# Performance work log

Measured on AMD Instinct MI355X. Metric: run time of the kernel, lower is better.

Reference implementation:

```python
import jax, jax.numpy as jnp
import numpy as np

DIM = 2048          # SDR dimension
CTX = 512           # top-down context (grid code) dimension
B = 8192            # batch of independent samples
N_PV = DIM // 4     # 512 PV interneurons
N_SV = DIM // 8     # 256 SOM/VIP interneurons
ALPHA_POS = 1.0 / 10.0   # dt / tau_pos
ALPHA_NEG = 1.0 / 10.0   # dt / tau_neg


def setup_inputs() -> dict:
    key = jax.random.key(0)
    ks = jax.random.split(key, 14)
    sc = 1.0 / np.sqrt(DIM)
    sc_sv = 1.0 / np.sqrt(N_SV)
    xav = np.sqrt(6.0 / (CTX + DIM))  # xavier uniform bound for predictor
    u = lambda k, shp, s: jax.random.uniform(k, shp, dtype=jnp.float32) * s
    return {
        "x_batch": jax.random.uniform(ks[0], (B, DIM), dtype=jnp.float32),
        "context_batch": jax.random.normal(ks[1], (B, CTX), dtype=jnp.float32),
        "r_pos_batch": jax.random.uniform(ks[2], (B, DIM), dtype=jnp.float32),
        "r_neg_batch": jax.random.uniform(ks[3], (B, DIM), dtype=jnp.float32),
        "W_pred": jax.random.uniform(ks[4], (DIM, CTX), jnp.float32, -xav, xav),
        "b_pred": jnp.zeros((DIM,), jnp.float32),
        "W_pv1_ff": u(ks[5], (N_PV, DIM), sc),
        "W_pv2_td": u(ks[6], (N_PV, DIM), sc),
        "W_vip_td": u(ks[7], (N_SV, DIM), sc),
        "W_som_in": u(ks[8], (N_SV, DIM), sc),
        "W_vip_som": u(ks[9], (N_SV, N_SV), sc_sv),
        "W_inh_pe_pos": u(ks[10], (DIM, N_PV), sc),
        "W_inh_pe_neg": u(ks[11], (DIM, N_PV), sc),
        "W_som_dend": u(ks[12], (DIM, N_SV), sc),
    }


def reference(x_batch, context_batch, r_pos_batch, r_neg_batch,
              W_pred, b_pred, W_pv1_ff, W_pv2_td, W_vip_td, W_som_in,
              W_vip_som, W_inh_pe_pos, W_inh_pe_neg, W_som_dend):
    relu = jax.nn.relu
    # top-down prediction: (B, CTX) @ (CTX, DIM) -> (B, DIM)
    predicted = context_batch @ W_pred.T + b_pred
    # interneuron circuit (Nemati 2025)
    r_pv1 = relu(x_batch @ W_pv1_ff.T)                               # (B, N_PV)
    r_pv2 = relu(predicted @ W_pv2_td.T)                             # (B, N_PV)
    r_vip = relu(predicted @ W_vip_td.T)                             # (B, N_SV)
    r_som = relu(relu(x_batch @ W_som_in.T) - r_vip @ W_vip_som.T)   # (B, N_SV)
    # signed prediction errors with somatic/dendritic inhibition
    pe_pos = relu(x_batch - predicted - r_pv2 @ W_inh_pe_pos.T)
    pe_neg = relu(predicted - x_batch - r_pv1 @ W_inh_pe_neg.T - r_som @ W_som_dend.T)
    # low-pass temporal filter of PE states
    new_r_pos = (1.0 - ALPHA_POS) * r_pos_batch + ALPHA_POS * pe_pos
    new_r_neg = (1.0 - ALPHA_NEG) * r_neg_batch + ALPHA_NEG * pe_neg
    return (new_r_pos, new_r_neg)
```

## Files before the change

kernel.cpp:

```cpp
#include <hip/hip_runtime.h>
#include <hip/hip_bf16.h>
#include <stdint.h>
#include <stddef.h>

#define DIMV 2048
#define CTXV 512
#define BV   8192
#define NPV  512
#define NSV  256

typedef __attribute__((ext_vector_type(8))) __bf16 bf16x8;
typedef __attribute__((ext_vector_type(4))) __bf16 bf16x4;
typedef __attribute__((ext_vector_type(4))) float f32x4;

__device__ __forceinline__ void gload_lds16(const void* g, void* l) {
    __builtin_amdgcn_global_load_lds(
        (const __attribute__((address_space(1))) unsigned int*)g,
        (__attribute__((address_space(3))) unsigned int*)l,
        16, 0, 0);
}

#define WAIT_VM8  asm volatile("s_waitcnt vmcnt(8)" ::: "memory")
#define WAIT_VM4  asm volatile("s_waitcnt vmcnt(4)" ::: "memory")
#define WAIT_VM0  asm volatile("s_waitcnt vmcnt(0)" ::: "memory")
#define WAIT_LGKM asm volatile("s_waitcnt lgkmcnt(0)" ::: "memory")
#define SBAR      __builtin_amdgcn_s_barrier()
#define SCHEDB    __builtin_amdgcn_sched_barrier(0)

struct CvtArgs {
    const float* src[11];
    __bf16*      dst[11];
};

__global__ __launch_bounds__(256) void cvt_all(CvtArgs a) {
    constexpr int NSEG = 11;
    constexpr unsigned cum[NSEG + 1] = {
        0u, 2097152u, 2621440u, 2752512u, 2883584u, 3014656u,
        3080192u, 3145728u, 3153920u, 3284992u, 3416064u, 3481600u};
    const unsigned total = cum[NSEG];
    for (unsigned c = blockIdx.x * blockDim.x + threadIdx.x; c < total;
         c += gridDim.x * blockDim.x) {
        const float* sp = a.src[0];
        __bf16*      dp = a.dst[0];
        unsigned     base = 0;
#pragma unroll
        for (int t = 1; t < NSEG; ++t) {
            const bool g = (c >= cum[t]);
            sp   = g ? a.src[t] : sp;
            dp   = g ? a.dst[t] : dp;
            base = g ? cum[t] : base;
        }
        const unsigned off = (c - base) * 8u;
        f32x4 v0 = *(const f32x4*)(sp + off);
        f32x4 v1 = *(const f32x4*)(sp + off + 4);
        bf16x8 o;
#pragma unroll
        for (int e = 0; e < 4; ++e) { o[e] = (__bf16)v0[e]; o[e + 4] = (__bf16)v1[e]; }
        *(bf16x8*)(dp + off) = o;
    }
}

__global__ __launch_bounds__(256)
void cvtT_wpred(const float* __restrict__ W, __bf16* __restrict__ WT) {
    __shared__ float t[64 * 65];
    const int bi  = blockIdx.x & 31;
    const int bj  = blockIdx.x >> 5;
    const int tid = threadIdx.x;
    const int tr  = tid >> 4;
    const int tc  = tid & 15;
#pragma unroll
    for (int rr = 0; rr < 4; ++rr) {
        const int r = tr + rr * 16;
        f32x4 v = *(const f32x4*)(W + (size_t)(bi * 64 + r) * 512 + bj * 64 + tc * 4);
#pragma unroll
        for (int e = 0; e < 4; ++e) t[(tc * 4 + e) * 65 + r] = v[e];
    }
    __syncthreads();
#pragma unroll
    for (int rr = 0; rr < 4; ++rr) {
        const int c = tr + rr * 16;
        bf16x4 o;
#pragma unroll
        for (int e = 0; e < 4; ++e) o[e] = (__bf16)t[c * 65 + tc * 4 + e];
        *(bf16x4*)(WT + (size_t)(bj * 64 + c) * 2048 + bi * 64 + tc * 4) = o;
    }
}

__global__ __launch_bounds__(512)
void bias_comb(const __bf16* __restrict__ Wpv2, const __bf16* __restrict__ Wvip,
               const float* __restrict__ b, float* __restrict__ out) {
    const int tid  = threadIdx.x;
    const int gw   = blockIdx.x * 8 + (tid >> 6);
    const int lane = tid & 63;
    const __bf16* row = (gw < 512) ? (Wpv2 + (size_t)gw * 2048)
                                   : (Wvip + (size_t)(gw - 512) * 2048);
    float acc = 0.f;
#pragma unroll
    for (int c = 0; c < 4; ++c) {
        const int j = lane * 32 + c * 8;
        bf16x8 w = *(const bf16x8*)(row + j);
        f32x4 b0 = *(const f32x4*)(b + j);
        f32x4 b1 = *(const f32x4*)(b + j + 4);
#pragma unroll
        for (int e = 0; e < 4; ++e) acc += (float)w[e] * b0[e];
#pragma unroll
        for (int e = 0; e < 4; ++e) acc += (float)w[e + 4] * b1[e];
    }
#pragma unroll
    for (int off = 32; off > 0; off >>= 1) acc += __shfl_down(acc, off);
    if (lane == 0) out[gw] = acc;
}

struct GemmDesc {
    const __bf16* A; int ldA;
    const __bf16* W1; const __bf16* W2; int ldW;
    int NB1;
    int N1cols, N2cols;
    int K, ntN;
    int epi;
    const float* bias;
    const __bf16* subp;
    void* out1; void* out2;
};

#define GEOM4                                                     \
    const int tid  = threadIdx.x;                                 \
    const int wave = tid >> 6;                                    \
    const int lane = tid & 63;                                    \
    const int lhi  = lane >> 4;                                   \
    const int llo  = lane & 15;                                   \
    const int wr   = wave >> 1;                                   \
    const int wc   = wave & 1;                                    \
    const int rins = lane >> 2;                                   \
    const int ch   = lane & 3;

#define LOAD_FRAGS5(BUF, af, bfr)                                     \
    _Pragma("unroll")                                                 \
    for (int i = 0; i < 4; ++i) {                                     \
        const int r  = wr * 64 + i * 16 + llo;                        \
        const int pc = lhi ^ ((r >> 1) & 3);                          \
        af[i] = *(const bf16x8*)(&ldsA[BUF][r * 64 + pc * 16]);       \
    }                                                                 \
    _Pragma("unroll")                                                 \
    for (int j = 0; j < 4; ++j) {                                     \
        const int r  = wc * 64 + j * 16 + llo;                        \
        const int pc = lhi ^ ((r >> 1) & 3);                          \
        bfr[j] = *(const bf16x8*)(&ldsB[BUF][r * 64 + pc * 16]);      \
    }

#define MFMA16(af, bfr, acc)                                                          \
    __builtin_amdgcn_s_setprio(1);                                                    \
    _Pragma("unroll")                                                                 \
    for (int i = 0; i < 4; ++i)                                                       \
        _Pragma("unroll")                                                             \
        for (int j = 0; j < 4; ++j)                                                   \
            acc[i][j] = __builtin_amdgcn_mfma_f32_16x16x32_bf16(bfr[j], af[i], acc[i][j], 0, 0, 0); \
    __builtin_amdgcn_s_setprio(0);

__global__ __launch_bounds__(256, 3)
void pe_gemm5(GemmDesc dA_, GemmDesc dB_, GemmDesc dC_, int s1, int s2)
{
    __shared__ __align__(16) char ldsA[3][8192];
    __shared__ __align__(16) char ldsB[3][8192];

    const int nwg = gridDim.x;
    const int bid = blockIdx.x;
    int wg = (bid & 7) * (nwg >> 3) + (bid >> 3);
    GemmDesc d = dA_;
    if (wg >= s2)      { d = dC_; wg -= s2; }
    else if (wg >= s1) { d = dB_; wg -= s1; }

    const int bx = wg / d.ntN;
    const int by = wg - bx * d.ntN;
    const int m0 = bx * 128;
    const int n0 = by * 128;

    const bool reg2  = (n0 >= d.NB1);
    const __bf16* Wc = reg2 ? d.W2 : d.W1;
    const int n0r    = reg2 ? (n0 - d.NB1) : n0;

    GEOM4

    const f32x4 fzero = {0.f, 0.f, 0.f, 0.f};
    f32x4 acc[4][4];
#pragma unroll
    for (int i = 0; i < 4; ++i)
#pragma unroll
        for (int j = 0; j < 4; ++j) acc[i][j] = fzero;

    const int nsteps = d.K >> 5;

#define STAGE5(S, BUF)                                                        \
    {                                                                         \
        const int kb_ = (S) * 32;                                             \
        _Pragma("unroll")                                                     \
        for (int half = 0; half < 2; ++half) {                                \
            const int rt = wave * 32 + half * 16 + rins;                      \
            const int kc = ch ^ ((rt >> 1) & 3);                              \
            const int kk = kb_ + kc * 8;                                      \
            gload_lds16(d.A + (size_t)(m0 + rt) * d.ldA + kk,                 \
                        &ldsA[BUF][wave * 2048 + half * 1024]);               \
            gload_lds16(Wc + (size_t)(n0r + rt) * d.ldW + kk,                 \
                        &ldsB[BUF][wave * 2048 + half * 1024]);               \
        }                                                                     \
    }

    STAGE5(0, 0)
    if (nsteps > 1) STAGE5(1, 1)
    for (int s = 0; s < nsteps; ++s) {
        if (s + 2 < nsteps) { STAGE5(s + 2, (s + 2) % 3) WAIT_VM8; }
        else if (s + 1 < nsteps) { WAIT_VM4; }
        else { WAIT_VM0; }
        SBAR;
        const int cb = s % 3;
        bf16x8 af[4], bfr[4];
        LOAD_FRAGS5(cb, af, bfr)
        MFMA16(af, bfr, acc)
        WAIT_LGKM; SCHEDB;
        SBAR;
    }
#undef STAGE5

#pragma unroll
    for (int i = 0; i < 4; ++i) {
#pragma unroll
        for (int j = 0; j < 4; ++j) {
            const int rowg = m0 + wr * 64 + i * 16 + llo;
            const int colb = wc * 64 + j * 16 + lhi * 4;
            if (d.epi == 0) {
                const size_t idx = (size_t)rowg * d.N1cols + (n0 + colb);
                f32x4 b4 = *(const f32x4*)(d.bias + n0 + colb);
                bf16x4 o;
#pragma unroll
                for (int r = 0; r < 4; ++r) o[r] = (__bf16)(acc[i][j][r] + b4[r]);
                *(bf16x4*)((__bf16*)d.out1 + idx) = o;
            } else if (d.epi == 1) {
                __bf16* op    = reg2 ? (__bf16*)d.out2 : (__bf16*)d.out1;
                const int ldo = reg2 ? d.N2cols : d.N1cols;
                const size_t idx = (size_t)rowg * ldo + (n0r + colb);
                bf16x4 o;
#pragma unroll
                for (int r = 0; r < 4; ++r) o[r] = (__bf16)fmaxf(acc[i][j][r], 0.f);
                *(bf16x4*)(op + idx) = o;
            } else if (d.epi == 2) {
                const size_t idx = (size_t)rowg * d.N1cols + (n0 + colb);
                bf16x4 s4 = *(const bf16x4*)(d.subp + idx);
                bf16x4 o;
#pragma unroll
                for (int r = 0; r < 4; ++r)
                    o[r] = (__bf16)fmaxf((float)s4[r] - acc[i][j][r], 0.f);
                *(bf16x4*)((__bf16*)d.out1 + idx) = o;
            } else if (d.epi == 3) {
                const size_t idx = (size_t)rowg * d.N1cols + (n0 + colb);
                bf16x4 o;
#pragma unroll
                for (int r = 0; r < 4; ++r) o[r] = (__bf16)acc[i][j][r];
                *(bf16x4*)((__bf16*)d.out1 + idx) = o;
            } else {
                __bf16* op    = reg2 ? (__bf16*)d.out2 : (__bf16*)d.out1;
                const int ldo = reg2 ? d.N2cols : d.N1cols;
                const size_t idx = (size_t)rowg * ldo + (n0r + colb);
                f32x4 b4 = *(const f32x4*)(d.bias + n0 + colb);
                bf16x4 o;
#pragma unroll
                for (int r = 0; r < 4; ++r)
                    o[r] = (__bf16)fmaxf(acc[i][j][r] + b4[r], 0.f);
                *(bf16x4*)(op + idx) = o;
            }
        }
    }
}

__global__ __launch_bounds__(256, 3)
void pe_filt5(const __bf16* __restrict__ rpv2, const __bf16* __restrict__ Wpepos,
              const __bf16* __restrict__ rpv1, const __bf16* __restrict__ rsom,
              const __bf16* __restrict__ Wpeneg, const __bf16* __restrict__ Wsomd,
              const __bf16* __restrict__ xbf, const __bf16* __restrict__ predb,
              const float* __restrict__ rpos, const float* __restrict__ rneg,
              float* __restrict__ outp, float* __restrict__ outn)
{
    __shared__ __align__(16) char ldsA[3][8192];
    __shared__ __align__(16) char ldsB[3][8192];

    const int nwg = gridDim.x;
    const int bid = blockIdx.x;
    const int wg  = (bid & 7) * (nwg >> 3) + (bid >> 3);
    const int bx  = wg >> 4;
    const int by  = wg & 15;
    const int m0  = bx * 128;
    const int n0  = by * 128;

    GEOM4

#define STAGE_F(Asrc, ldAv, Wsrc, ldWv, KB, BUF)                              \
    {                                                                         \
        _Pragma("unroll")                                                     \
        for (int half = 0; half < 2; ++half) {                                \
            const int rt = wave * 32 + half * 16 + rins;                      \
            const int kc = ch ^ ((rt >> 1) & 3);                              \
            const int kk = (KB) + kc * 8;                                     \
            gload_lds16((Asrc) + (size_t)(m0 + rt) * (ldAv) + kk,             \
                        &ldsA[BUF][wave * 2048 + half * 1024]);               \
            gload_lds16((Wsrc) + (size_t)(n0 + rt) * (ldWv) + kk,             \
                        &ldsB[BUF][wave * 2048 + half * 1024]);               \
        }                                                                     \
    }
#define STAGE_NEG(S, BUF)                                                     \
    {                                                                         \
        if ((S) < 16) { STAGE_F(rpv1, NPV, Wpeneg, NPV, (S) * 32, BUF) }      \
        else          { STAGE_F(rsom, NSV, Wsomd, NSV, ((S) - 16) * 32, BUF) }\
    }

    const f32x4 fzero = {0.f, 0.f, 0.f, 0.f};
    f32x4 acc[4][4];
#pragma unroll
    for (int i = 0; i < 4; ++i)
#pragma unroll
        for (int j = 0; j < 4; ++j) acc[i][j] = fzero;

    STAGE_F(rpv2, NPV, Wpepos, NPV, 0, 0)
    STAGE_F(rpv2, NPV, Wpepos, NPV, 32, 1)
    for (int s = 0; s < 16; ++s) {
        if (s + 2 < 16) { STAGE_F(rpv2, NPV, Wpepos, NPV, (s + 2) * 32, (s + 2) % 3) WAIT_VM8; }
        else if (s + 1 < 16) { WAIT_VM4; }
        else { WAIT_VM0; }
        SBAR;
        const int cb = s % 3;
        bf16x8 af[4], bfr[4];
        LOAD_FRAGS5(cb, af, bfr)
        MFMA16(af, bfr, acc)
        WAIT_LGKM; SCHEDB;
        SBAR;
    }
    STAGE_NEG(0, 0)
    STAGE_NEG(1, 1)

#pragma unroll
    for (int i = 0; i < 4; ++i) {
#pragma unroll
        for (int j = 0; j < 4; ++j) {
            const int rowg = m0 + wr * 64 + i * 16 + llo;
            const int colg = n0 + wc * 64 + j * 16 + lhi * 4;
            const size_t idx = (size_t)rowg * 2048 + colg;
            f32x4 rp  = *(const f32x4*)(rpos + idx);
            bf16x4 xb = *(const bf16x4*)(xbf + idx);
            bf16x4 pb = *(const bf16x4*)(predb + idx);
            f32x4 o;
#pragma unroll
            for (int r = 0; r < 4; ++r) {
                const float dd = (float)xb[r] - (float)pb[r];
                o[r] = 0.9f * rp[r] + 0.1f * fmaxf(dd - acc[i][j][r], 0.f);
            }
            *(f32x4*)(outp + idx) = o;
            acc[i][j] = fzero;
        }
    }

    for (int s = 0; s < 24; ++s) {
        if (s + 2 < 24) { STAGE_NEG(s + 2, (s + 2) % 3) WAIT_VM8; }
        else if (s + 1 < 24) { WAIT_VM4; }
        else { WAIT_VM0; }
        SBAR;
        const int cb = s % 3;
        bf16x8 af[4], bfr[4];
        LOAD_FRAGS5(cb, af, bfr)
        MFMA16(af, bfr, acc)
        WAIT_LGKM; SCHEDB;
        SBAR;
    }

#pragma unroll
    for (int i = 0; i < 4; ++i) {
#pragma unroll
        for (int j = 0; j < 4; ++j) {
            const int rowg = m0 + wr * 64 + i * 16 + llo;
            const int colg = n0 + wc * 64 + j * 16 + lhi * 4;
            const size_t idx = (size_t)rowg * 2048 + colg;
            f32x4 rn  = *(const f32x4*)(rneg + idx);
            bf16x4 xb = *(const bf16x4*)(xbf + idx);
            bf16x4 pb = *(const bf16x4*)(predb + idx);
            f32x4 o;
#pragma unroll
            for (int r = 0; r < 4; ++r) {
                const float dd = (float)pb[r] - (float)xb[r];
                o[r] = 0.9f * rn[r] + 0.1f * fmaxf(dd - acc[i][j][r], 0.f);
            }
            *(f32x4*)(outn + idx) = o;
        }
    }
#undef STAGE_NEG
#undef STAGE_F
}

extern "C" void kernel_launch(void* const* d_in, const int* in_sizes, int n_in,
                              void* d_out, int out_size, void* d_ws, size_t ws_size,
                              hipStream_t stream) {
    (void)in_sizes; (void)n_in; (void)out_size; (void)ws_size;

    const float* x       = (const float*)d_in[0];
    const float* ctx     = (const float*)d_in[1];
    const float* r_pos   = (const float*)d_in[2];
    const float* r_neg   = (const float*)d_in[3];
    const float* Wpred   = (const float*)d_in[4];
    const float* bpred   = (const float*)d_in[5];
    const float* Wpv1    = (const float*)d_in[6];
    const float* Wpv2    = (const float*)d_in[7];
    const float* Wvip    = (const float*)d_in[8];
    const float* Wsomin  = (const float*)d_in[9];
    const float* Wvipsom = (const float*)d_in[10];
    const float* Wpepos  = (const float*)d_in[11];
    const float* Wpeneg  = (const float*)d_in[12];
    const float* Wsomd   = (const float*)d_in[13];

    char* ws = (char*)d_ws;
    __bf16* x_bf      = (__bf16*)ws; ws += (size_t)BV * DIMV * 2;
    __bf16* ctx_bf    = (__bf16*)ws; ws += (size_t)BV * CTXV * 2;
    __bf16* pred_bf   = (__bf16*)ws; ws += (size_t)BV * DIMV * 2;
    __bf16* rpv1_bf   = (__bf16*)ws; ws += (size_t)BV * NPV * 2;
    __bf16* rpv2_bf   = (__bf16*)ws; ws += (size_t)BV * NPV * 2;
    __bf16* rvip_bf   = (__bf16*)ws; ws += (size_t)BV * NSV * 2;
    __bf16* ssom_bf   = (__bf16*)ws; ws += (size_t)BV * NSV * 2;
    __bf16* rsom_bf   = (__bf16*)ws; ws += (size_t)BV * NSV * 2;
    __bf16* Wpred_bf  = (__bf16*)ws; ws += (size_t)DIMV * CTXV * 2;
    __bf16* Wpv1_bf   = (__bf16*)ws; ws += (size_t)NPV * DIMV * 2;
    __bf16* Wpv2_bf   = (__bf16*)ws; ws += (size_t)NPV * DIMV * 2;
    __bf16* Wvip_bf   = (__bf16*)ws; ws += (size_t)NSV * DIMV * 2;
    __bf16* Wsomin_bf = (__bf16*)ws; ws += (size_t)NSV * DIMV * 2;
    __bf16* Wvipsom_bf= (__bf16*)ws; ws += (size_t)NSV * NSV * 2;
    __bf16* Wpepos_bf = (__bf16*)ws; ws += (size_t)DIMV * NPV * 2;
    __bf16* Wpeneg_bf = (__bf16*)ws; ws += (size_t)DIMV * NPV * 2;
    __bf16* Wsomd_bf  = (__bf16*)ws; ws += (size_t)DIMV * NSV * 2;
    __bf16* WpredT_bf = (__bf16*)ws; ws += (size_t)CTXV * DIMV * 2;
    __bf16* Wcomb2    = (__bf16*)ws; ws += (size_t)NPV * CTXV * 2;
    __bf16* Wcombv    = (__bf16*)ws; ws += (size_t)NSV * CTXV * 2;
    float*  biascomb  = (float*)ws;  ws += 768 * 4;

    float* out_pos = (float*)d_out;
    float* out_neg = out_pos + (size_t)BV * DIMV;

    CvtArgs ca;
    ca.src[0] = x;       ca.dst[0] = x_bf;
    ca.src[1] = ctx;     ca.dst[1] = ctx_bf;
    ca.src[2] = Wpred;   ca.dst[2] = Wpred_bf;
    ca.src[3] = Wpv1;    ca.dst[3] = Wpv1_bf;
    ca.src[4] = Wpv2;    ca.dst[4] = Wpv2_bf;
    ca.src[5] = Wvip;    ca.dst[5] = Wvip_bf;
    ca.src[6] = Wsomin;  ca.dst[6] = Wsomin_bf;
    ca.src[7] = Wvipsom; ca.dst[7] = Wvipsom_bf;
    ca.src[8] = Wpepos;  ca.dst[8] = Wpepos_bf;
    ca.src[9] = Wpeneg;  ca.dst[9] = Wpeneg_bf;
    ca.src[10] = Wsomd;  ca.dst[10] = Wsomd_bf;
    cvt_all<<<dim3(2048), dim3(256), 0, stream>>>(ca);
    cvtT_wpred<<<dim3(256), dim3(256), 0, stream>>>(Wpred, WpredT_bf);
    bias_comb<<<dim3(96), dim3(512), 0, stream>>>(Wpv2_bf, Wvip_bf, bpred, biascomb);

    const int BIG = 1 << 28;
    GemmDesc dz;
    dz.A = nullptr; dz.ldA = 0; dz.W1 = dz.W2 = nullptr; dz.ldW = 0;
    dz.NB1 = BIG; dz.N1cols = dz.N2cols = 0; dz.K = 32; dz.ntN = 1;
    dz.epi = 3; dz.bias = nullptr; dz.subp = nullptr;
    dz.out1 = dz.out2 = nullptr;

    GemmDesc d_pred = dz;
    d_pred.A = ctx_bf; d_pred.ldA = CTXV;
    d_pred.W1 = d_pred.W2 = Wpred_bf; d_pred.ldW = CTXV;
    d_pred.K = CTXV; d_pred.ntN = 16; d_pred.N1cols = DIMV; d_pred.epi = 0;
    d_pred.bias = bpred; d_pred.out1 = pred_bf;

    GemmDesc d_c2 = dz;
    d_c2.A = Wpv2_bf; d_c2.ldA = DIMV;
    d_c2.W1 = d_c2.W2 = WpredT_bf; d_c2.ldW = DIMV;
    d_c2.K = DIMV; d_c2.ntN = 4; d_c2.N1cols = CTXV; d_c2.epi = 3;
    d_c2.out1 = Wcomb2;

    GemmDesc d_cv = d_c2;
    d_cv.A = Wvip_bf;
    d_cv.out1 = Wcombv;

    pe_gemm5<<<dim3(1048), dim3(256), 0, stream>>>(d_pred, d_c2, d_cv, 1024, 1040);

    GemmDesc d_23 = dz;
    d_23.A = x_bf; d_23.ldA = DIMV;
    d_23.W1 = Wpv1_bf; d_23.W2 = Wsomin_bf; d_23.ldW = DIMV;
    d_23.K = DIMV; d_23.ntN = 6; d_23.NB1 = NPV;
    d_23.N1cols = NPV; d_23.N2cols = NSV; d_23.epi = 1;
    d_23.out1 = rpv1_bf; d_23.out2 = ssom_bf;

    GemmDesc d_45 = dz;
    d_45.A = ctx_bf; d_45.ldA = CTXV;
    d_45.W1 = Wcomb2; d_45.W2 = Wcombv; d_45.ldW = CTXV;
    d_45.K = CTXV; d_45.ntN = 6; d_45.NB1 = NPV;
    d_45.N1cols = NPV; d_45.N2cols = NSV; d_45.epi = 4;
    d_45.bias = biascomb; d_45.out1 = rpv2_bf; d_45.out2 = rvip_bf;

    pe_gemm5<<<dim3(768), dim3(256), 0, stream>>>(d_23, d_45, dz, 384, 768);

    GemmDesc d_som = dz;
    d_som.A = rvip_bf; d_som.ldA = NSV;
    d_som.W1 = d_som.W2 = Wvipsom_bf; d_som.ldW = NSV;
    d_som.K = NSV; d_som.ntN = 2; d_som.N1cols = NSV; d_som.epi = 2;
    d_som.subp = ssom_bf; d_som.out1 = rsom_bf;

    pe_gemm5<<<dim3(128), dim3(256), 0, stream>>>(d_som, d_som, d_som, 128, 128);

    pe_filt5<<<dim3(1024), dim3(256), 0, stream>>>(
        rpv2_bf, Wpepos_bf, rpv1_bf, rsom_bf, Wpeneg_bf, Wsomd_bf,
        x_bf, pred_bf, r_pos, r_neg, out_pos, out_neg);
}
```

Before: 313.7 us.

## Use single barrier per K-step with asm LDS reads in triple-buffered GEMM loops

Restructures the triple-buffered K loops so each step waits on the oldest prefetch, takes one barrier, then issues the next global-to-LDS prefetch before reading fragments. The trailing barrier is removed, which the 3-buffer rotation allows because the buffer being overwritten was consumed two steps earlier. LDS fragment reads become inline-asm ds_read_b128 followed by an lgkmcnt wait before the MFMAs. This aims to halve barrier overhead per step, at the cost of less compiler freedom to interleave LDS reads with MFMAs and a shallower vmcnt wait window.

After: 306.1 us. 2.4% less time.

```diff
diff --git a/kernel.cpp b/kernel.cpp
--- a/kernel.cpp
+++ b/kernel.cpp
@@ -12,6 +12,8 @@
 typedef __attribute__((ext_vector_type(8))) __bf16 bf16x8;
 typedef __attribute__((ext_vector_type(4))) __bf16 bf16x4;
 typedef __attribute__((ext_vector_type(4))) float f32x4;
+typedef __attribute__((ext_vector_type(4))) int   i32x4;
+typedef __attribute__((address_space(3))) const char* lds_cp;
 
 __device__ __forceinline__ void gload_lds16(const void* g, void* l) {
     __builtin_amdgcn_global_load_lds(
@@ -20,7 +22,12 @@
         16, 0, 0);
 }
 
-#define WAIT_VM8  asm volatile("s_waitcnt vmcnt(8)" ::: "memory")
+__device__ __forceinline__ bf16x8 lds_read16(const char* p) {
+    i32x4 r;
+    asm volatile("ds_read_b128 %0, %1" : "=v"(r) : "v"((lds_cp)p));
+    return __builtin_bit_cast(bf16x8, r);
+}
+
 #define WAIT_VM4  asm volatile("s_waitcnt vmcnt(4)" ::: "memory")
 #define WAIT_VM0  asm volatile("s_waitcnt vmcnt(0)" ::: "memory")
 #define WAIT_LGKM asm volatile("s_waitcnt lgkmcnt(0)" ::: "memory")
@@ -134,18 +141,18 @@
     const int rins = lane >> 2;                                   \
     const int ch   = lane & 3;
 
-#define LOAD_FRAGS5(BUF, af, bfr)                                     \
+#define LOAD_FRAGS_ASM(BUF, af, bfr)                                  \
     _Pragma("unroll")                                                 \
     for (int i = 0; i < 4; ++i) {                                     \
         const int r  = wr * 64 + i * 16 + llo;                        \
         const int pc = lhi ^ ((r >> 1) & 3);                          \
-        af[i] = *(const bf16x8*)(&ldsA[BUF][r * 64 + pc * 16]);       \
+        af[i] = lds_read16(&ldsA[BUF][r * 64 + pc * 16]);             \
     }                                                                 \
     _Pragma("unroll")                                                 \
     for (int j = 0; j < 4; ++j) {                                     \
         const int r  = wc * 64 + j * 16 + llo;                        \
         const int pc = lhi ^ ((r >> 1) & 3);                          \
-        bfr[j] = *(const bf16x8*)(&ldsB[BUF][r * 64 + pc * 16]);      \
+        bfr[j] = lds_read16(&ldsB[BUF][r * 64 + pc * 16]);            \
     }
 
 #define MFMA16(af, bfr, acc)                                                          \
@@ -208,16 +215,13 @@
     STAGE5(0, 0)
     if (nsteps > 1) STAGE5(1, 1)
     for (int s = 0; s < nsteps; ++s) {
-        if (s + 2 < nsteps) { STAGE5(s + 2, (s + 2) % 3) WAIT_VM8; }
-        else if (s + 1 < nsteps) { WAIT_VM4; }
-        else { WAIT_VM0; }
+        if (s + 1 < nsteps) { WAIT_VM4; } else { WAIT_VM0; }
         SBAR;
-        const int cb = s % 3;
+        if (s + 2 < nsteps) STAGE5(s + 2, (s + 2) % 3)
         bf16x8 af[4], bfr[4];
-        LOAD_FRAGS5(cb, af, bfr)
+        LOAD_FRAGS_ASM(s % 3, af, bfr)
+        WAIT_LGKM; SCHEDB;
         MFMA16(af, bfr, acc)
-        WAIT_LGKM; SCHEDB;
-        SBAR;
     }
 #undef STAGE5
 
@@ -321,17 +325,15 @@
     STAGE_F(rpv2, NPV, Wpepos, NPV, 0, 0)
     STAGE_F(rpv2, NPV, Wpepos, NPV, 32, 1)
     for (int s = 0; s < 16; ++s) {
-        if (s + 2 < 16) { STAGE_F(rpv2, NPV, Wpepos, NPV, (s + 2) * 32, (s + 2) % 3) WAIT_VM8; }
-        else if (s + 1 < 16) { WAIT_VM4; }
-        else { WAIT_VM0; }
+        if (s + 1 < 16) { WAIT_VM4; } else { WAIT_VM0; }
         SBAR;
-        const int cb = s % 3;
+        if (s + 2 < 16) STAGE_F(rpv2, NPV, Wpepos, NPV, (s + 2) * 32, (s + 2) % 3)
         bf16x8 af[4], bfr[4];
-        LOAD_FRAGS5(cb, af, bfr)
+        LOAD_FRAGS_ASM(s % 3, af, bfr)
+        WAIT_LGKM; SCHEDB;
         MFMA16(af, bfr, acc)
-        WAIT_LGKM; SCHEDB;
-        SBAR;
-    }
+    }
+    SBAR;
     STAGE_NEG(0, 0)
     STAGE_NEG(1, 1)
 
@@ -357,16 +359,13 @@
     }
 
     for (int s = 0; s < 24; ++s) {
-        if (s + 2 < 24) { STAGE_NEG(s + 2, (s + 2) % 3) WAIT_VM8; }
-        else if (s + 1 < 24) { WAIT_VM4; }
-        else { WAIT_VM0; }
+        if (s + 1 < 24) { WAIT_VM4; } else { WAIT_VM0; }
         SBAR;
-        const int cb = s % 3;
+        if (s + 2 < 24) STAGE_NEG(s + 2, (s + 2) % 3)
         bf16x8 af[4], bfr[4];
-        LOAD_FRAGS5(cb, af, bfr)
+        LOAD_FRAGS_ASM(s % 3, af, bfr)
+        WAIT_LGKM; SCHEDB;
         MFMA16(af, bfr, acc)
-        WAIT_LGKM; SCHEDB;
-        SBAR;
     }
 
 #pragma unroll
```
